# Kernel optimization log

Measured on AMD Instinct MI355X. Metric: run time of the kernel, lower is better.

The kernel has to match this reference:

```python
import jax, jax.numpy as jnp
import numpy as np

EPS = 1e-7          # keras.backend.epsilon()
L2_EPS = 1e-12      # tf.math.l2_normalize epsilon


def _l2_normalize(v):
    # tf.math.l2_normalize: v * rsqrt(max(sum(v^2), 1e-12))
    sq = jnp.sum(v * v, axis=-1, keepdims=True)
    return v * jax.lax.rsqrt(jnp.maximum(sq, L2_EPS))


def setup_inputs() -> dict:
    key = jax.random.key(0)
    k1, k2 = jax.random.split(key)
    x = jax.random.normal(k1, (4, 2048, 1024), dtype=jnp.float32)
    ref = jax.random.normal(k2, (8192, 1024), dtype=jnp.float32)
    return {"x": x, "ref": ref}


def reference(x, ref):
    # inputs += K.epsilon()
    xn = _l2_normalize(x + EPS)          # [B, N, D]
    refn = _l2_normalize(ref)            # [M, D]
    # fused form of sum(xn[..., N, 1, D] * refn[1, M, D], axis=-1) -> [B, N, M]
    return jnp.einsum('bnd,md->bnm', xn, refn)
```

## Files before the change

### kernel.cpp

```cpp
#include <hip/hip_runtime.h>
#include <hip/hip_bf16.h>
#include <stdint.h>

typedef __bf16 bf16x8 __attribute__((ext_vector_type(8)));
typedef float f32x4 __attribute__((ext_vector_type(4)));

#define GLB_AS __attribute__((address_space(1)))
#define LDS_AS __attribute__((address_space(3)))

__device__ __forceinline__ void gload_lds16(const void* g, void* l) {
    __builtin_amdgcn_global_load_lds((GLB_AS void*)(g), (LDS_AS void*)(l), 16, 0, 0);
}

#define GM 8192
#define GN 8192
#define GK 1024
#define NT (GK / 64)
#define NI (NT / 2)

__global__ __launch_bounds__(256) void normalize_rows(
    const float* __restrict__ x, const float* __restrict__ ref,
    __bf16* __restrict__ outA, __bf16* __restrict__ outB)
{
    const int row = blockIdx.x;
    const bool isX = row < 8192;
    const size_t r = isX ? (size_t)row : (size_t)(row - 8192);
    const float* src = isX ? (x + r * 1024) : (ref + r * 1024);
    __bf16* dst = isX ? (outA + r * 1024) : (outB + r * 1024);
    const float eps = isX ? 1e-7f : 0.0f;

    const int t = threadIdx.x;
    float4 v = reinterpret_cast<const float4*>(src)[t];
    v.x += eps; v.y += eps; v.z += eps; v.w += eps;
    float ss = v.x * v.x + v.y * v.y + v.z * v.z + v.w * v.w;

    #pragma unroll
    for (int o = 32; o; o >>= 1) ss += __shfl_xor(ss, o, 64);

    __shared__ float red[4];
    const int wv = t >> 6, lane = t & 63;
    if (lane == 0) red[wv] = ss;
    __syncthreads();
    const float tot = red[0] + red[1] + red[2] + red[3];
    const float inv = rsqrtf(fmaxf(tot, 1e-12f));

    __bf16 b[4];
    b[0] = (__bf16)(v.x * inv);
    b[1] = (__bf16)(v.y * inv);
    b[2] = (__bf16)(v.z * inv);
    b[3] = (__bf16)(v.w * inv);
    uint2 pk;
    __builtin_memcpy(&pk, b, 8);
    reinterpret_cast<uint2*>(dst)[t] = pk;
}

__global__ __launch_bounds__(512, 2) void gemm_bt8(
    const __bf16* __restrict__ A, const __bf16* __restrict__ B,
    float* __restrict__ C)
{
    __shared__ __bf16 As[2][2][128][64];
    __shared__ __bf16 Bs[2][2][128][64];

    const int bid = blockIdx.x;
    const int g  = bid >> 8;
    const int x  = bid & 7;
    const int ii = (bid >> 3) & 31;
    const int tm = (g & 1) * 16 + (x & 3) * 4 + (ii & 3);
    const int tn = (g >> 1) * 16 + (x >> 2) * 8 + (ii >> 2);
    const size_t rowM0 = (size_t)tm * 256;
    const size_t rowN0 = (size_t)tn * 256;

    const int tid  = threadIdx.x;
    const int wave = tid >> 6;
    const int lane = tid & 63;
    const int wr = wave >> 2;
    const int wc = wave & 3;

    const int srow  = lane >> 3;
    const int sslot = (lane & 7) ^ srow;
    const int fr = lane & 15;
    const int fs = lane >> 4;

    bf16x8 af[4][2];
    bf16x8 bq[2][2][2];
    f32x4  acc[8][4] = {};

#define STAGE_A(T, h, b) { \
    _Pragma("unroll") \
    for (int j = 0; j < 2; ++j) { \
        const size_t grow = rowM0 + (size_t)(j) * 128 + (h) * 64 + wave * 8 + srow; \
        const char* src = (const char*)A + (grow * GK + (size_t)(T) * 64) * 2 + sslot * 16; \
        char* dst = (char*)&As[b][h][0][0] + (j * 64 + wave * 8) * 128; \
        gload_lds16(src, dst); } }

#define STAGE_B(T, h, b) { \
    _Pragma("unroll") \
    for (int j = 0; j < 2; ++j) { \
        const int l = j * 64 + wave * 8 + srow; \
        const size_t grow = rowN0 + (size_t)(l >> 5) * 64 + (h) * 32 + (l & 31); \
        const char* src = (const char*)B + (grow * GK + (size_t)(T) * 64) * 2 + sslot * 16; \
        char* dst = (char*)&Bs[b][h][0][0] + (j * 64 + wave * 8) * 128; \
        gload_lds16(src, dst); } }

#define LDA(qm, b) { \
    _Pragma("unroll") \
    for (int m = 0; m < 4; ++m) { \
        const int l = wr * 64 + m * 16 + fr; \
        _Pragma("unroll") \
        for (int ks = 0; ks < 2; ++ks) { \
            const int slot = (ks * 4 + fs) ^ (l & 7); \
            af[m][ks] = *(const bf16x8*)((const char*)&As[b][qm][0][0] + l * 128 + slot * 16); } } }

#define LDB(qn, b) { \
    _Pragma("unroll") \
    for (int n = 0; n < 2; ++n) { \
        const int l = wc * 32 + n * 16 + fr; \
        _Pragma("unroll") \
        for (int ks = 0; ks < 2; ++ks) { \
            const int slot = (ks * 4 + fs) ^ (l & 7); \
            bq[qn][n][ks] = *(const bf16x8*)((const char*)&Bs[b][qn][0][0] + l * 128 + slot * 16); } } }

#define QMFMA(qm, qn) { \
    __builtin_amdgcn_s_setprio(1); \
    _Pragma("unroll") \
    for (int ks = 0; ks < 2; ++ks) \
    _Pragma("unroll") \
    for (int m = 0; m < 4; ++m) \
    _Pragma("unroll") \
    for (int n = 0; n < 2; ++n) \
        acc[(qm) * 4 + m][(qn) * 2 + n] = __builtin_amdgcn_mfma_f32_16x16x32_bf16( \
            bq[qn][n][ks], af[m][ks], acc[(qm) * 4 + m][(qn) * 2 + n], 0, 0, 0); \
    __builtin_amdgcn_s_setprio(0); }

#define STORE_QUAD(qm, qn) { \
    _Pragma("unroll") \
    for (int m = 0; m < 4; ++m) \
    _Pragma("unroll") \
    for (int n = 0; n < 2; ++n) { \
        const size_t row = rowM0 + (size_t)wr * 128 + (qm) * 64 + m * 16 + (lane & 15); \
        const size_t col = rowN0 + (size_t)wc * 64 + (qn) * 32 + n * 16 + (lane >> 4) * 4; \
        *reinterpret_cast<f32x4*>(&C[row * (size_t)GN + col]) = acc[(qm) * 4 + m][(qn) * 2 + n]; } }

#define BAR() __builtin_amdgcn_s_barrier()
#define WAIT_LGKM0() { asm volatile("s_waitcnt lgkmcnt(0)" ::: "memory"); __builtin_amdgcn_sched_barrier(0); }
#define WAIT_VM(n)   { asm volatile("s_waitcnt vmcnt(" #n ")" ::: "memory"); __builtin_amdgcn_sched_barrier(0); }

    STAGE_A(0, 0, 0); STAGE_A(0, 1, 0); STAGE_B(0, 0, 0); STAGE_B(0, 1, 0);
    STAGE_A(1, 0, 1); STAGE_B(1, 0, 1); STAGE_B(1, 1, 1);
    WAIT_VM(6);
    BAR();

    #pragma unroll 1
    for (int i = 0; i < NI; ++i) {
        const int t1 = 2 * i + 1, t2 = 2 * i + 2, t3 = 2 * i + 3;
        const bool more = (i < NI - 1);

        LDA(0, 0); LDB(0, 0);
        STAGE_A(t1, 1, 1);
        BAR(); WAIT_LGKM0();
        QMFMA(0, 0);
        BAR();
        LDB(1, 0);
        if (more) STAGE_A(t2, 0, 0);
        BAR(); WAIT_LGKM0();
        QMFMA(0, 1);
        BAR();
        LDA(1, 0);
        if (more) STAGE_B(t2, 0, 0);
        BAR(); WAIT_LGKM0();
        QMFMA(1, 0);
        BAR();
        if (more) { STAGE_B(t2, 1, 0); WAIT_VM(6); }
        else      { WAIT_VM(0); }
        BAR();
        QMFMA(1, 1);
        BAR();
        LDA(0, 1); LDB(0, 1);
        if (more) STAGE_A(t2, 1, 0);
        BAR(); WAIT_LGKM0();
        QMFMA(0, 0);
        if (!more) STORE_QUAD(0, 0);
        BAR();
        LDB(1, 1);
        if (more) STAGE_A(t3, 0, 1);
        BAR(); WAIT_LGKM0();
        QMFMA(0, 1);
        if (!more) STORE_QUAD(0, 1);
        BAR();
        LDA(1, 1);
        if (more) STAGE_B(t3, 0, 1);
        BAR(); WAIT_LGKM0();
        QMFMA(1, 0);
        if (!more) STORE_QUAD(1, 0);
        BAR();
        if (more) {
            STAGE_B(t3, 1, 1); WAIT_VM(6);
            BAR();
            QMFMA(1, 1);
            BAR();
        } else {
            BAR();
            QMFMA(1, 1);
            STORE_QUAD(1, 1);
        }
    }

#undef STAGE_A
#undef STAGE_B
#undef LDA
#undef LDB
#undef QMFMA
#undef STORE_QUAD
#undef BAR
#undef WAIT_LGKM0
#undef WAIT_VM
}

__global__ __launch_bounds__(256) void naive_pairwise(
    const float* __restrict__ x, const float* __restrict__ ref,
    float* __restrict__ out)
{
    const int row = blockIdx.x >> 5;
    const int j = (blockIdx.x & 31) * 256 + threadIdx.x;
    const float* xr = x + (size_t)row * 1024;
    const float* rr = ref + (size_t)j * 1024;

    __shared__ float xs[1024];
    float part = 0.f;
    for (int k = threadIdx.x; k < 1024; k += 256) {
        float v = xr[k] + 1e-7f;
        xs[k] = v;
        part += v * v;
    }
    #pragma unroll
    for (int o = 32; o; o >>= 1) part += __shfl_xor(part, o, 64);
    __shared__ float red[4];
    if ((threadIdx.x & 63) == 0) red[threadIdx.x >> 6] = part;
    __syncthreads();
    const float ssx = red[0] + red[1] + red[2] + red[3];

    float ssr = 0.f, dot = 0.f;
    for (int k = 0; k < 1024; ++k) {
        float r = rr[k];
        ssr += r * r;
        dot += r * xs[k];
    }
    out[(size_t)row * 8192 + j] =
        dot * rsqrtf(fmaxf(ssx, 1e-12f)) * rsqrtf(fmaxf(ssr, 1e-12f));
}

extern "C" void kernel_launch(void* const* d_in, const int* in_sizes, int n_in,
                              void* d_out, int out_size, void* d_ws, size_t ws_size,
                              hipStream_t stream) {
    const float* x   = (const float*)d_in[0];
    const float* ref = (const float*)d_in[1];
    float* out = (float*)d_out;

    const size_t need = (size_t)GM * GK * sizeof(__bf16) * 2;
    if (ws_size >= need) {
        __bf16* wsA = (__bf16*)d_ws;
        __bf16* wsB = wsA + (size_t)GM * GK;
        normalize_rows<<<16384, 256, 0, stream>>>(x, ref, wsA, wsB);
        gemm_bt8<<<(GM / 256) * (GN / 256), 512, 0, stream>>>(wsA, wsB, out);
    } else {
        naive_pairwise<<<8192 * 32, 256, 0, stream>>>(x, ref, out);
    }
}
```

Baseline: 179.8 us.

## Make GEMM persistent: each block computes four 256x256 tiles in a 512x512 region

Replaces the 1024-block GEMM launch with 256 persistent blocks, each iterating over four 256x256 output tiles of a 512x512 super-tile. The K-loop prefetch pipeline now flows across tile boundaries, so the first stages of the next tile load while the previous tile's epilogue stores run. Accumulators are reset with zero-init MFMAs on each tile's first step. The aim is to remove block launch and prologue overhead and the tail effects between waves of blocks. In exchange there are fewer blocks in flight, the stores become serialized inside each block, and the vmcnt accounting at tile boundaries is more complex.

```diff
diff --git a/kernel.cpp b/kernel.cpp
--- a/kernel.cpp
+++ b/kernel.cpp
@@ -15,8 +15,6 @@
 #define GM 8192
 #define GN 8192
 #define GK 1024
-#define NT (GK / 64)
-#define NI (NT / 2)
 
 __global__ __launch_bounds__(256) void normalize_rows(
     const float* __restrict__ x, const float* __restrict__ ref,
@@ -54,7 +52,7 @@
     reinterpret_cast<uint2*>(dst)[t] = pk;
 }
 
-__global__ __launch_bounds__(512, 2) void gemm_bt8(
+__global__ __launch_bounds__(512, 2) void gemm_pers(
     const __bf16* __restrict__ A, const __bf16* __restrict__ B,
     float* __restrict__ C)
 {
@@ -62,13 +60,11 @@
     __shared__ __bf16 Bs[2][2][128][64];
 
     const int bid = blockIdx.x;
-    const int g  = bid >> 8;
-    const int x  = bid & 7;
-    const int ii = (bid >> 3) & 31;
-    const int tm = (g & 1) * 16 + (x & 3) * 4 + (ii & 3);
-    const int tn = (g >> 1) * 16 + (x >> 2) * 8 + (ii >> 2);
-    const size_t rowM0 = (size_t)tm * 256;
-    const size_t rowN0 = (size_t)tn * 256;
+    const int xcd = bid & 7, sq = bid >> 3;
+    const int u = (xcd & 3) * 4 + (sq & 3);
+    const int v = (xcd >> 2) * 8 + (sq >> 2);
+    const size_t u0 = (size_t)u * 512;
+    const size_t v0 = (size_t)v * 512;
 
     const int tid  = threadIdx.x;
     const int wave = tid >> 6;
@@ -85,20 +81,25 @@
     bf16x8 bq[2][2][2];
     f32x4  acc[8][4] = {};
 
-#define STAGE_A(T, h, b) { \
+#define BASE_M(q) (u0 + ((((q) >> 4) == 1 || ((q) >> 4) == 2) ? 256 : 0))
+#define BASE_N(q) (v0 + ((((q) >> 4) >= 2) ? 256 : 0))
+
+#define STAGE_A(rM, q, h, b) { \
+    const size_t kcol = (size_t)((q) & 15) * 64; \
     _Pragma("unroll") \
     for (int j = 0; j < 2; ++j) { \
-        const size_t grow = rowM0 + (size_t)(j) * 128 + (h) * 64 + wave * 8 + srow; \
-        const char* src = (const char*)A + (grow * GK + (size_t)(T) * 64) * 2 + sslot * 16; \
+        const size_t grow = (rM) + (size_t)(j) * 128 + (h) * 64 + wave * 8 + srow; \
+        const char* src = (const char*)A + (grow * GK + kcol) * 2 + sslot * 16; \
         char* dst = (char*)&As[b][h][0][0] + (j * 64 + wave * 8) * 128; \
         gload_lds16(src, dst); } }
 
-#define STAGE_B(T, h, b) { \
+#define STAGE_B(rN, q, h, b) { \
+    const size_t kcol = (size_t)((q) & 15) * 64; \
     _Pragma("unroll") \
     for (int j = 0; j < 2; ++j) { \
         const int l = j * 64 + wave * 8 + srow; \
-        const size_t grow = rowN0 + (size_t)(l >> 5) * 64 + (h) * 32 + (l & 31); \
-        const char* src = (const char*)B + (grow * GK + (size_t)(T) * 64) * 2 + sslot * 16; \
+        const size_t grow = (rN) + (size_t)(l >> 5) * 64 + (h) * 32 + (l & 31); \
+        const char* src = (const char*)B + (grow * GK + kcol) * 2 + sslot * 16; \
         char* dst = (char*)&Bs[b][h][0][0] + (j * 64 + wave * 8) * 128; \
         gload_lds16(src, dst); } }
 
@@ -132,84 +133,112 @@
             bq[qn][n][ks], af[m][ks], acc[(qm) * 4 + m][(qn) * 2 + n], 0, 0, 0); \
     __builtin_amdgcn_s_setprio(0); }
 
-#define STORE_QUAD(qm, qn) { \
+#define QMFMA_F(qm, qn) { \
+    __builtin_amdgcn_s_setprio(1); \
+    _Pragma("unroll") \
+    for (int m = 0; m < 4; ++m) \
+    _Pragma("unroll") \
+    for (int n = 0; n < 2; ++n) \
+        acc[(qm) * 4 + m][(qn) * 2 + n] = __builtin_amdgcn_mfma_f32_16x16x32_bf16( \
+            bq[qn][n][0], af[m][0], (f32x4){0.f, 0.f, 0.f, 0.f}, 0, 0, 0); \
+    _Pragma("unroll") \
+    for (int m = 0; m < 4; ++m) \
+    _Pragma("unroll") \
+    for (int n = 0; n < 2; ++n) \
+        acc[(qm) * 4 + m][(qn) * 2 + n] = __builtin_amdgcn_mfma_f32_16x16x32_bf16( \
+            bq[qn][n][1], af[m][1], acc[(qm) * 4 + m][(qn) * 2 + n], 0, 0, 0); \
+    __builtin_amdgcn_s_setprio(0); }
+
+#define STORE_QUAD(qm, qn, rM, rN) { \
     _Pragma("unroll") \
     for (int m = 0; m < 4; ++m) \
     _Pragma("unroll") \
     for (int n = 0; n < 2; ++n) { \
-        const size_t row = rowM0 + (size_t)wr * 128 + (qm) * 64 + m * 16 + (lane & 15); \
-        const size_t col = rowN0 + (size_t)wc * 64 + (qn) * 32 + n * 16 + (lane >> 4) * 4; \
+        const size_t row = (rM) + (size_t)wr * 128 + (qm) * 64 + m * 16 + (lane & 15); \
+        const size_t col = (rN) + (size_t)wc * 64 + (qn) * 32 + n * 16 + (lane >> 4) * 4; \
         *reinterpret_cast<f32x4*>(&C[row * (size_t)GN + col]) = acc[(qm) * 4 + m][(qn) * 2 + n]; } }
 
 #define BAR() __builtin_amdgcn_s_barrier()
 #define WAIT_LGKM0() { asm volatile("s_waitcnt lgkmcnt(0)" ::: "memory"); __builtin_amdgcn_sched_barrier(0); }
 #define WAIT_VM(n)   { asm volatile("s_waitcnt vmcnt(" #n ")" ::: "memory"); __builtin_amdgcn_sched_barrier(0); }
 
-    STAGE_A(0, 0, 0); STAGE_A(0, 1, 0); STAGE_B(0, 0, 0); STAGE_B(0, 1, 0);
-    STAGE_A(1, 0, 1); STAGE_B(1, 0, 1); STAGE_B(1, 1, 1);
+    STAGE_A(u0, 0, 0, 0); STAGE_A(u0, 0, 1, 0); STAGE_B(v0, 0, 0, 0); STAGE_B(v0, 0, 1, 0);
+    STAGE_A(u0, 1, 0, 1); STAGE_B(v0, 1, 0, 1); STAGE_B(v0, 1, 1, 1);
     WAIT_VM(6);
     BAR();
 
     #pragma unroll 1
-    for (int i = 0; i < NI; ++i) {
-        const int t1 = 2 * i + 1, t2 = 2 * i + 2, t3 = 2 * i + 3;
-        const bool more = (i < NI - 1);
+    for (int i = 0; i < 32; ++i) {
+        const int q1 = 2 * i + 1, q2 = 2 * i + 2, q3 = 2 * i + 3;
+        const bool more  = (i < 31);
+        const bool first = (i & 7) == 0;
+        const bool lastt = (i & 7) == 7;
+        const int  tj = i >> 3;
+        const size_t rMs = u0 + ((tj == 1 || tj == 2) ? 256 : 0);
+        const size_t rNs = v0 + ((tj >= 2) ? 256 : 0);
+        const size_t rM2 = BASE_M(q2), rN2 = BASE_N(q2);
+        const size_t rM3 = BASE_M(q3), rN3 = BASE_N(q3);
 
         LDA(0, 0); LDB(0, 0);
-        STAGE_A(t1, 1, 1);
+        STAGE_A(rMs, q1, 1, 1);
+        BAR(); WAIT_LGKM0();
+        if (first) { QMFMA_F(0, 0); } else { QMFMA(0, 0); }
+        BAR();
+        LDB(1, 0);
+        if (more) STAGE_A(rM2, q2, 0, 0);
+        BAR(); WAIT_LGKM0();
+        if (first) { QMFMA_F(0, 1); } else { QMFMA(0, 1); }
+        BAR();
+        LDA(1, 0);
+        if (more) STAGE_B(rN2, q2, 0, 0);
+        BAR(); WAIT_LGKM0();
+        if (first) { QMFMA_F(1, 0); } else { QMFMA(1, 0); }
+        BAR();
+        if (more) { STAGE_B(rN2, q2, 1, 0); WAIT_VM(6); }
+        else      { WAIT_VM(0); }
+        BAR();
+        if (first) { QMFMA_F(1, 1); } else { QMFMA(1, 1); }
+        BAR();
+        LDA(0, 1); LDB(0, 1);
+        if (more) STAGE_A(rM2, q2, 1, 0);
         BAR(); WAIT_LGKM0();
         QMFMA(0, 0);
-        BAR();
-        LDB(1, 0);
-        if (more) STAGE_A(t2, 0, 0);
+        if (lastt) STORE_QUAD(0, 0, rMs, rNs);
+        BAR();
+        LDB(1, 1);
+        if (more) STAGE_A(rM3, q3, 0, 1);
         BAR(); WAIT_LGKM0();
         QMFMA(0, 1);
-        BAR();
-        LDA(1, 0);
-        if (more) STAGE_B(t2, 0, 0);
+        if (lastt) STORE_QUAD(0, 1, rMs, rNs);
+        BAR();
+        LDA(1, 1);
+        if (more) STAGE_B(rN3, q3, 0, 1);
         BAR(); WAIT_LGKM0();
         QMFMA(1, 0);
-        BAR();
-        if (more) { STAGE_B(t2, 1, 0); WAIT_VM(6); }
-        else      { WAIT_VM(0); }
-        BAR();
-        QMFMA(1, 1);
-        BAR();
-        LDA(0, 1); LDB(0, 1);
-        if (more) STAGE_A(t2, 1, 0);
-        BAR(); WAIT_LGKM0();
-        QMFMA(0, 0);
-        if (!more) STORE_QUAD(0, 0);
-        BAR();
-        LDB(1, 1);
-        if (more) STAGE_A(t3, 0, 1);
-        BAR(); WAIT_LGKM0();
-        QMFMA(0, 1);
-        if (!more) STORE_QUAD(0, 1);
-        BAR();
-        LDA(1, 1);
-        if (more) STAGE_B(t3, 0, 1);
-        BAR(); WAIT_LGKM0();
-        QMFMA(1, 0);
-        if (!more) STORE_QUAD(1, 0);
+        if (lastt) STORE_QUAD(1, 0, rMs, rNs);
         BAR();
         if (more) {
-            STAGE_B(t3, 1, 1); WAIT_VM(6);
+            STAGE_B(rN3, q3, 1, 1);
+            if (lastt) { WAIT_VM(38); } else { WAIT_VM(6); }
             BAR();
             QMFMA(1, 1);
+            if (lastt) STORE_QUAD(1, 1, rMs, rNs);
             BAR();
         } else {
             BAR();
             QMFMA(1, 1);
-            STORE_QUAD(1, 1);
+            STORE_QUAD(1, 1, rMs, rNs);
         }
     }
 
+#undef BASE_M
+#undef BASE_N
 #undef STAGE_A
 #undef STAGE_B
 #undef LDA
 #undef LDB
 #undef QMFMA
+#undef QMFMA_F
 #undef STORE_QUAD
 #undef BAR
 #undef WAIT_LGKM0
@@ -261,7 +290,7 @@
         __bf16* wsA = (__bf16*)d_ws;
         __bf16* wsB = wsA + (size_t)GM * GK;
         normalize_rows<<<16384, 256, 0, stream>>>(x, ref, wsA, wsB);
-        gemm_bt8<<<(GM / 256) * (GN / 256), 512, 0, stream>>>(wsA, wsB, out);
+        gemm_pers<<<256, 512, 0, stream>>>(wsA, wsB, out);
     } else {
         naive_pairwise<<<8192 * 32, 256, 0, stream>>>(x, ref, out);
     }
```

Result: slower. 183.5 us (+2.1%).

## Rework GEMM tile swizzle, precompute LDS offsets, relax waitcnt fences, defer stores

Applied to the files above, without the earlier changes.

Replaces the block-to-tile mapping with an XCD-aware swizzle that groups 4x4 tiles per super-block, so neighbouring blocks on one die share A/B rows in L2. LDS fragment offsets are computed once per thread instead of on every load. The waitcnt macros drop their sched_barrier and memory clobbers and add a partial lgkmcnt(8) wait before the barrier, giving the compiler more freedom to interleave LDS reads with MFMA. The output stores are moved after the loop. Without the sched_barriers and memory clobbers, the compiler may reorder loads across the waits, which risks correctness or a worse schedule.

```diff
diff --git a/kernel.cpp b/kernel.cpp
--- a/kernel.cpp
+++ b/kernel.cpp
@@ -54,7 +54,7 @@
     reinterpret_cast<uint2*>(dst)[t] = pk;
 }
 
-__global__ __launch_bounds__(512, 2) void gemm_bt8(
+__global__ __launch_bounds__(512, 2) void gemm_v9(
     const __bf16* __restrict__ A, const __bf16* __restrict__ B,
     float* __restrict__ C)
 {
@@ -62,11 +62,11 @@
     __shared__ __bf16 Bs[2][2][128][64];
 
     const int bid = blockIdx.x;
-    const int g  = bid >> 8;
-    const int x  = bid & 7;
-    const int ii = (bid >> 3) & 31;
-    const int tm = (g & 1) * 16 + (x & 3) * 4 + (ii & 3);
-    const int tn = (g >> 1) * 16 + (x >> 2) * 8 + (ii >> 2);
+    const int swz = (bid & 7) * 128 + (bid >> 3);
+    const int within = swz & 15;
+    const int super  = swz >> 4;
+    const int tm = (super & 7) * 4 + (within & 3);
+    const int tn = (super >> 3) * 4 + (within >> 2);
     const size_t rowM0 = (size_t)tm * 256;
     const size_t rowN0 = (size_t)tn * 256;
 
@@ -80,6 +80,22 @@
     const int sslot = (lane & 7) ^ srow;
     const int fr = lane & 15;
     const int fs = lane >> 4;
+
+    int woffA[4][2], woffB[2][2];
+    #pragma unroll
+    for (int m = 0; m < 4; ++m) {
+        const int l = wr * 64 + m * 16 + fr;
+        #pragma unroll
+        for (int ks = 0; ks < 2; ++ks)
+            woffA[m][ks] = l * 128 + (((ks * 4 + fs) ^ (l & 7)) * 16);
+    }
+    #pragma unroll
+    for (int n = 0; n < 2; ++n) {
+        const int l = wc * 32 + n * 16 + fr;
+        #pragma unroll
+        for (int ks = 0; ks < 2; ++ks)
+            woffB[n][ks] = l * 128 + (((ks * 4 + fs) ^ (l & 7)) * 16);
+    }
 
     bf16x8 af[4][2];
     bf16x8 bq[2][2][2];
@@ -104,21 +120,17 @@
 
 #define LDA(qm, b) { \
     _Pragma("unroll") \
-    for (int m = 0; m < 4; ++m) { \
-        const int l = wr * 64 + m * 16 + fr; \
-        _Pragma("unroll") \
-        for (int ks = 0; ks < 2; ++ks) { \
-            const int slot = (ks * 4 + fs) ^ (l & 7); \
-            af[m][ks] = *(const bf16x8*)((const char*)&As[b][qm][0][0] + l * 128 + slot * 16); } } }
+    for (int m = 0; m < 4; ++m) \
+    _Pragma("unroll") \
+    for (int ks = 0; ks < 2; ++ks) \
+        af[m][ks] = *(const bf16x8*)((const char*)&As[b][qm][0][0] + woffA[m][ks]); }
 
 #define LDB(qn, b) { \
     _Pragma("unroll") \
-    for (int n = 0; n < 2; ++n) { \
-        const int l = wc * 32 + n * 16 + fr; \
-        _Pragma("unroll") \
-        for (int ks = 0; ks < 2; ++ks) { \
-            const int slot = (ks * 4 + fs) ^ (l & 7); \
-            bq[qn][n][ks] = *(const bf16x8*)((const char*)&Bs[b][qn][0][0] + l * 128 + slot * 16); } } }
+    for (int n = 0; n < 2; ++n) \
+    _Pragma("unroll") \
+    for (int ks = 0; ks < 2; ++ks) \
+        bq[qn][n][ks] = *(const bf16x8*)((const char*)&Bs[b][qn][0][0] + woffB[n][ks]); }
 
 #define QMFMA(qm, qn) { \
     __builtin_amdgcn_s_setprio(1); \
@@ -142,12 +154,13 @@
         *reinterpret_cast<f32x4*>(&C[row * (size_t)GN + col]) = acc[(qm) * 4 + m][(qn) * 2 + n]; } }
 
 #define BAR() __builtin_amdgcn_s_barrier()
-#define WAIT_LGKM0() { asm volatile("s_waitcnt lgkmcnt(0)" ::: "memory"); __builtin_amdgcn_sched_barrier(0); }
-#define WAIT_VM(n)   { asm volatile("s_waitcnt vmcnt(" #n ")" ::: "memory"); __builtin_amdgcn_sched_barrier(0); }
+#define LGKM8()  asm volatile("s_waitcnt lgkmcnt(8)")
+#define LGKM0()  asm volatile("s_waitcnt lgkmcnt(0)")
+#define VM(n)    asm volatile("s_waitcnt vmcnt(" #n ")" ::: "memory")
 
     STAGE_A(0, 0, 0); STAGE_A(0, 1, 0); STAGE_B(0, 0, 0); STAGE_B(0, 1, 0);
     STAGE_A(1, 0, 1); STAGE_B(1, 0, 1); STAGE_B(1, 1, 1);
-    WAIT_VM(6);
+    VM(6);
     BAR();
 
     #pragma unroll 1
@@ -157,53 +170,52 @@
 
         LDA(0, 0); LDB(0, 0);
         STAGE_A(t1, 1, 1);
-        BAR(); WAIT_LGKM0();
+        LGKM8();
+        BAR(); LGKM0();
         QMFMA(0, 0);
         BAR();
         LDB(1, 0);
         if (more) STAGE_A(t2, 0, 0);
-        BAR(); WAIT_LGKM0();
+        BAR(); LGKM0();
         QMFMA(0, 1);
         BAR();
         LDA(1, 0);
         if (more) STAGE_B(t2, 0, 0);
-        BAR(); WAIT_LGKM0();
+        BAR(); LGKM0();
         QMFMA(1, 0);
         BAR();
-        if (more) { STAGE_B(t2, 1, 0); WAIT_VM(6); }
-        else      { WAIT_VM(0); }
+        if (more) { STAGE_B(t2, 1, 0); VM(6); }
+        else      { VM(0); }
         BAR();
         QMFMA(1, 1);
         BAR();
         LDA(0, 1); LDB(0, 1);
         if (more) STAGE_A(t2, 1, 0);
-        BAR(); WAIT_LGKM0();
+        LGKM8();
+        BAR(); LGKM0();
         QMFMA(0, 0);
-        if (!more) STORE_QUAD(0, 0);
         BAR();
         LDB(1, 1);
         if (more) STAGE_A(t3, 0, 1);
-        BAR(); WAIT_LGKM0();
+        BAR(); LGKM0();
         QMFMA(0, 1);
-        if (!more) STORE_QUAD(0, 1);
         BAR();
         LDA(1, 1);
         if (more) STAGE_B(t3, 0, 1);
-        BAR(); WAIT_LGKM0();
+        BAR(); LGKM0();
         QMFMA(1, 0);
-        if (!more) STORE_QUAD(1, 0);
         BAR();
         if (more) {
-            STAGE_B(t3, 1, 1); WAIT_VM(6);
+            STAGE_B(t3, 1, 1); VM(6);
             BAR();
             QMFMA(1, 1);
             BAR();
         } else {
-            BAR();
             QMFMA(1, 1);
-            STORE_QUAD(1, 1);
         }
     }
+
+    STORE_QUAD(0, 0); STORE_QUAD(0, 1); STORE_QUAD(1, 0); STORE_QUAD(1, 1);
 
 #undef STAGE_A
 #undef STAGE_B
@@ -212,8 +224,9 @@
 #undef QMFMA
 #undef STORE_QUAD
 #undef BAR
-#undef WAIT_LGKM0
-#undef WAIT_VM
+#undef LGKM8
+#undef LGKM0
+#undef VM
 }
 
 __global__ __launch_bounds__(256) void naive_pairwise(
@@ -261,7 +274,7 @@
         __bf16* wsA = (__bf16*)d_ws;
         __bf16* wsB = wsA + (size_t)GM * GK;
         normalize_rows<<<16384, 256, 0, stream>>>(x, ref, wsA, wsB);
-        gemm_bt8<<<(GM / 256) * (GN / 256), 512, 0, stream>>>(wsA, wsB, out);
+        gemm_v9<<<(GM / 256) * (GN / 256), 512, 0, stream>>>(wsA, wsB, out);
     } else {
         naive_pairwise<<<8192 * 32, 256, 0, stream>>>(x, ref, out);
     }
```

New measurement: 185.9 us. +3.4%, slower.
